# Kernel optimization log

Hardware: AMD Instinct MI355X
Metric: run time of the kernel (lower is better)

Reference implementation:

```python
import jax, jax.numpy as jnp
import numpy as np
from jax.scipy.special import logsumexp

B, L = 32, 128
NEG = -1e9
SPAN_LAMB = 0.5


def setup_inputs() -> dict:
    key = jax.random.key(0)
    ks = jax.random.split(key, 8)
    span_logits = jax.random.normal(ks[0], (B, L, L, 2), jnp.float32)
    ph = jax.random.normal(ks[1], (B, L, L), jnp.float32)
    pt = jax.random.normal(ks[2], (B, L, L), jnp.float32)
    ph_arc = jax.random.normal(ks[3], (B, L, L), jnp.float32)
    spans_ind = jax.random.randint(ks[4], (B, L, L), 0, 3, jnp.int32)
    ph_ind = jax.random.randint(ks[5], (B, L, L), 0, 2, jnp.int32)
    pt_ind = jax.random.randint(ks[6], (B, L, L), 0, 2, jnp.int32)
    lens = jax.random.randint(ks[7], (B,), L // 2, L + 1, jnp.int32)
    i = jnp.arange(L)
    # maskspan[b,i,j] = valid right-closed span i..j within sentence b; row 0 sums to lens
    maskspan = (i[None, :, None] <= i[None, None, :]) & (i[None, None, :] < lens[:, None, None])
    maskarc = (i[None, :, None] < lens[:, None, None]) & (i[None, None, :] < lens[:, None, None])
    return dict(span_logits=span_logits, ph=ph, pt=pt, ph_arc=ph_arc,
                spans_ind=spans_ind, ph_ind=ph_ind, pt_ind=pt_ind,
                maskspan=maskspan, maskarc=maskarc)


def _inside_logZ(span_logits, lens):
    # CYK inside algorithm over right-closed spans; returns sum_b logZ_b.
    scores = logsumexp(span_logits, axis=-1)  # [B,L,L] span score = lse over labels
    Ln = scores.shape[1]
    ar = jnp.arange(Ln)
    # width-0 base: s[i,i] = scores[i,i]
    s0 = jnp.where(jnp.eye(Ln, dtype=bool)[None], scores, NEG)
    li = ar[:, None] + ar[None, :]        # [L,L]: left child right end i+k
    ri = li + 1                           # right child left end i+k+1
    li_c = jnp.clip(li, 0, Ln - 1)
    ri_c = jnp.clip(ri, 0, Ln - 1)

    def step(s, w):
        j = ar + w
        jc = jnp.clip(j, 0, Ln - 1)
        left = s[:, ar[:, None], li_c]                 # [B,L,L] left[b,i,k]=s[b,i,i+k]
        right = s[:, ri_c, jc[:, None]]                # right[b,i,k]=s[b,i+k+1,i+w]
        comb = jnp.where(ar[None, None, :] < w, left + right, NEG)
        new = scores[:, ar, jc] + logsumexp(comb, axis=-1)  # [B,L]
        valid = (j < Ln)[None, :]
        cur = s[:, ar, jc]
        s = s.at[:, ar, jc].set(jnp.where(valid, new, cur))
        return s, None

    s, _ = jax.lax.scan(step, s0, jnp.arange(1, Ln))
    logZ = jnp.take_along_axis(s[:, 0, :], (lens - 1)[:, None], axis=1)[:, 0]
    return logZ.sum()


def _bce_mean(x, y, m):
    # stable BCEWithLogits, mean over masked elements
    l = jnp.maximum(x, 0.0) - x * y + jnp.log1p(jnp.exp(-jnp.abs(x)))
    return jnp.where(m, l, 0.0).sum() / m.sum().astype(jnp.float32)


def reference(span_logits, ph, pt, ph_arc, spans_ind, ph_ind, pt_ind, maskspan, maskarc):
    lens = maskspan[:, 0].sum(-1)                         # [B]
    spans_b = jnp.where(spans_ind > 0, spans_ind - 1, spans_ind).astype(bool)
    # label marginals = d logZ / d span_logits (matches torch autograd-based cyk)
    marginals = jax.grad(_inside_logZ)(span_logits, lens)  # [B,L,L,2]
    pos_mask = maskspan & spans_b
    neg_mask = maskspan & (~spans_b)
    pos_loss = jnp.log(jnp.where(pos_mask, jnp.maximum(marginals[..., 1], 1e-38), 1.0)).sum()
    neg_loss = jnp.log(jnp.where(neg_mask, jnp.maximum(marginals[..., 0], 1e-38), 1.0)).sum()
    loss_spans = -(pos_loss + neg_loss) / lens.sum().astype(jnp.float32)
    loss_ph = _bce_mean(ph, ph_ind.astype(jnp.float32), maskarc)
    loss_pt = _bce_mean(pt, pt_ind.astype(jnp.float32), maskarc)
    return SPAN_LAMB * loss_spans + (1.0 - SPAN_LAMB) * (loss_ph + loss_pt)
```

## Files before the change

### kernel.cpp

```cpp
#include <hip/hip_runtime.h>
#include <hip/hip_bf16.h>
#include <float.h>

#define NB 32
#define NBCE 32
#define L 128
#define NT 1024
#define R 132
#define PAD 40
#define LOGMIN -87.49823f

__device__ __forceinline__ int mask_mode(const void* p) {
    unsigned int v = ((const unsigned int*)p)[0];
    if (v == 1u) return 1;
    if (v == 0x3F800000u) return 2;
    return 0;
}
__device__ __forceinline__ bool mask_at(const void* p, int mode, int idx) {
    if (mode == 1) return ((const int*)p)[idx] != 0;
    if (mode == 2) return ((const float*)p)[idx] != 0.0f;
    return ((const unsigned char*)p)[idx] != 0;
}

__device__ __forceinline__ float lse2(float a, float b) {
    return fmaxf(a, b) + log1pf(__expf(-fabsf(a - b)));
}

template<int C>
__device__ __forceinline__ float dppf(float x) {
    return __int_as_float(__builtin_amdgcn_mov_dpp(__float_as_int(x), C, 0xF, 0xF, true));
}
template<int T>
__device__ __forceinline__ float bfly_max(float x) {
    x = fmaxf(x, dppf<0xB1>(x));
    x = fmaxf(x, dppf<0x4E>(x));
    x = fmaxf(x, dppf<0x141>(x));
    if (T == 16) x = fmaxf(x, dppf<0x140>(x));
    return x;
}
template<int T>
__device__ __forceinline__ float bfly_add(float x) {
    x += dppf<0xB1>(x);
    x += dppf<0x4E>(x);
    x += dppf<0x141>(x);
    if (T == 16) x += dppf<0x140>(x);
    return x;
}

template<int T, int NUMAX>
__device__ __forceinline__ void load_terms(float* v, int sub, int nterm,
                                           const float* p1, const float* p2, float& mloc) {
    p1 += sub; p2 += sub;
#pragma unroll
    for (int kk = 0; kk < NUMAX; kk += 2) {
        if (kk * T >= nterm) break;
        const int o0 = kk * T, o1 = o0 + T;
        float a0 = p1[o0] + p2[o0];
        float a1 = p1[o1] + p2[o1];
        a0 = (sub + o0 < nterm) ? a0 : -FLT_MAX;
        a1 = (sub + o1 < nterm) ? a1 : -FLT_MAX;
        v[kk] = a0; v[kk + 1] = a1;
        mloc = fmaxf(mloc, fmaxf(a0, a1));
    }
}
template<int T, int NUMAX>
__device__ __forceinline__ void sum_exp(const float* v, int nterm, float M, float& s) {
#pragma unroll
    for (int kk = 0; kk < NUMAX; kk += 2) {
        if (kk * T >= nterm) break;
        s += __expf(v[kk] - M) + __expf(v[kk + 1] - M);
    }
}

__global__ __launch_bounds__(NT, 1) void tree_dp_kernel(
    const float* __restrict__ logits,
    const int*   __restrict__ spans_ind,
    const void*  __restrict__ maskspan,
    const float* __restrict__ ph, const float* __restrict__ pt,
    const int* __restrict__ ph_ind, const int* __restrict__ pt_ind,
    const void* __restrict__ maskarc,
    double*      __restrict__ ws)
{
    const int tid = threadIdx.x;

    if (blockIdx.x >= NB) {
        const int mode = mask_mode(maskarc);
        const int tot = NB * L * L;
        double sph = 0.0, spt = 0.0, cnt = 0.0;
        for (int idx = (blockIdx.x - NB) * NT + tid; idx < tot; idx += NBCE * NT) {
            if (mask_at(maskarc, mode, idx)) {
                float x = ph[idx]; float y = (float)ph_ind[idx];
                sph += (double)(fmaxf(x, 0.0f) - x * y + log1pf(__expf(-fabsf(x))));
                x = pt[idx]; y = (float)pt_ind[idx];
                spt += (double)(fmaxf(x, 0.0f) - x * y + log1pf(__expf(-fabsf(x))));
                cnt += 1.0;
            }
        }
        for (int off = 32; off > 0; off >>= 1) {
            sph += __shfl_down(sph, off);
            spt += __shfl_down(spt, off);
            cnt += __shfl_down(cnt, off);
        }
        if ((tid & 63) == 0) {
            atomicAdd(&ws[2], sph); atomicAdd(&ws[3], spt); atomicAdd(&ws[4], cnt);
        }
        return;
    }

    __shared__ float Am[L * R + PAD];
    __shared__ float Gm[L * R + PAD];

    const int b = blockIdx.x;
    const int mbase = b * L * L;
    const int mode = mask_mode(maskspan);

    int pred = (tid < L) && mask_at(maskspan, mode, mbase + tid);
    const int n = __syncthreads_count(pred);

    const float* lg = logits + (size_t)b * L * L * 2;

    for (int e = tid; e < L * L; e += NT) {
        int i = e >> 7, j = e & (L - 1);
        if (i <= j && j < n) {
            const float* p = lg + (size_t)e * 2;
            float v = lse2(p[0], p[1]);
            Am[i * R + j] = v; Am[j * R + i] = v;
            Gm[i * R + j] = v; Gm[j * R + i] = v;
        }
    }
    __syncthreads();

    for (int w = 1; w < n; ++w) {
        int c = n - w;
        if (c > 64) {
            int cell = tid >> 3, sub = tid & 7;
            if (cell < c) {
                int i = cell, j = i + w;
                float v[8]; float mloc = -FLT_MAX;
                load_terms<8, 8>(v, sub, w, &Am[i * R + i], &Am[j * R + i + 1], mloc);
                float M = bfly_max<8>(mloc);
                float s = 0.0f;
                sum_exp<8, 8>(v, w, M, s);
                float S = bfly_add<8>(s);
                if (sub == 0) {
                    float val = Am[i * R + j] + M + __logf(S);
                    Am[i * R + j] = val; Am[j * R + i] = val;
                }
            }
        } else {
            int cell = tid >> 4, sub = tid & 15;
            if (cell < c) {
                int i = cell, j = i + w;
                float v[8]; float mloc = -FLT_MAX;
                load_terms<16, 8>(v, sub, w, &Am[i * R + i], &Am[j * R + i + 1], mloc);
                float M = bfly_max<16>(mloc);
                float s = 0.0f;
                sum_exp<16, 8>(v, w, M, s);
                float S = bfly_add<16>(s);
                if (sub == 0) {
                    float val = Am[i * R + j] + M + __logf(S);
                    Am[i * R + j] = val; Am[j * R + i] = val;
                }
            }
        }
        __syncthreads();
    }

    const float logZ = Am[n - 1];

    for (int w = n - 2; w >= 1; --w) {
        int c = n - w;
        if (c > 64) {
            int cell = tid >> 3, sub = tid & 7;
            if (cell < c) {
                int i = cell, j = i + w;
                int nt1 = n - 1 - j;
                float v1[16], v2[16]; float mloc = -FLT_MAX;
                load_terms<8, 16>(v1, sub, nt1, &Gm[i * R + j + 1], &Am[(j + 1) * R + j + 1], mloc);
                load_terms<8, 16>(v2, sub, i,   &Gm[j * R],         &Am[(i - 1) * R],         mloc);
                float M = bfly_max<8>(mloc);
                float s = 0.0f;
                sum_exp<8, 16>(v1, nt1, M, s);
                sum_exp<8, 16>(v2, i,   M, s);
                float S = bfly_add<8>(s);
                if (sub == 0) {
                    float val = Gm[i * R + j] + M + __logf(S);
                    Gm[i * R + j] = val; Gm[j * R + i] = val;
                }
            }
        } else {
            int cell = tid >> 4, sub = tid & 15;
            if (cell < c) {
                int i = cell, j = i + w;
                int nt1 = n - 1 - j;
                float v1[4], v2[4]; float mloc = -FLT_MAX;
                load_terms<16, 4>(v1, sub, nt1, &Gm[i * R + j + 1], &Am[(j + 1) * R + j + 1], mloc);
                load_terms<16, 4>(v2, sub, i,   &Gm[j * R],         &Am[(i - 1) * R],         mloc);
                float M = bfly_max<16>(mloc);
                float s = 0.0f;
                sum_exp<16, 4>(v1, nt1, M, s);
                sum_exp<16, 4>(v2, i,   M, s);
                float S = bfly_add<16>(s);
                if (sub == 0) {
                    float val = Gm[i * R + j] + M + __logf(S);
                    Gm[i * R + j] = val; Gm[j * R + i] = val;
                }
            }
        }
        __syncthreads();
    }

    const int* si = spans_ind + mbase;
    double local = 0.0;
    {
        int cell = tid >> 3, sub = tid & 7;
        if (cell < n) {
            int i = cell;
            int nt1 = n - 1 - i;
            float v1[16], v2[16]; float mloc = -FLT_MAX;
            load_terms<8, 16>(v1, sub, nt1, &Gm[i * R + i + 1], &Am[(i + 1) * R + i + 1], mloc);
            load_terms<8, 16>(v2, sub, i,   &Gm[i * R],         &Am[(i - 1) * R],         mloc);
            float M = bfly_max<8>(mloc);
            float s = 0.0f;
            sum_exp<8, 16>(v1, nt1, M, s);
            sum_exp<8, 16>(v2, i,   M, s);
            float S = bfly_add<8>(s);
            if (sub == 0) {
                float beta_ii = M + __logf(S);
                const float* p = lg + ((size_t)i * L + i) * 2;
                int ind = si[i * L + i];
                float lc = (ind == 2) ? p[1] : p[0];
                float logm = beta_ii - logZ + lc;
                local += (double)fmaxf(logm, LOGMIN);
            }
        }
    }

    for (int e = tid; e < L * L; e += NT) {
        int i = e >> 7, j = e & (L - 1);
        if (i < j && j < n) {
            const float* p = lg + (size_t)e * 2;
            float a = p[0], cc = p[1];
            float sc = lse2(a, cc);
            int ind = si[e];
            float lc = (ind == 2) ? cc : a;
            float logm = Am[i * R + j] + Gm[i * R + j] - logZ + lc - 2.0f * sc;
            local += (double)fmaxf(logm, LOGMIN);
        }
    }

    for (int off = 32; off > 0; off >>= 1)
        local += __shfl_down(local, off);
    if ((tid & 63) == 0) atomicAdd(&ws[0], local);
    if (tid == 0) atomicAdd(&ws[1], (double)n);
}

__global__ void finalize_kernel(const double* __restrict__ ws, float* __restrict__ out) {
    double loss_spans = -ws[0] / ws[1];
    double bce = (ws[2] + ws[3]) / ws[4];
    out[0] = (float)(0.5 * loss_spans + 0.5 * bce);
}

extern "C" void kernel_launch(void* const* d_in, const int* in_sizes, int n_in,
                              void* d_out, int out_size, void* d_ws, size_t ws_size,
                              hipStream_t stream) {
    (void)in_sizes; (void)n_in; (void)out_size; (void)ws_size;
    const float* span_logits = (const float*)d_in[0];
    const float* ph          = (const float*)d_in[1];
    const float* pt          = (const float*)d_in[2];
    const int*   spans_ind   = (const int*)d_in[4];
    const int*   ph_ind      = (const int*)d_in[5];
    const int*   pt_ind      = (const int*)d_in[6];
    const void*  maskspan    = d_in[7];
    const void*  maskarc     = d_in[8];
    double* ws = (double*)d_ws;
    float* out = (float*)d_out;

    hipMemsetAsync(d_ws, 0, 5 * sizeof(double), stream);
    hipLaunchKernelGGL(tree_dp_kernel, dim3(NB + NBCE), dim3(NT), 0, stream,
                       span_logits, spans_ind, maskspan,
                       ph, pt, ph_ind, pt_ind, maskarc, ws);
    hipLaunchKernelGGL(finalize_kernel, dim3(1), dim3(1), 0, stream, ws, out);
}
```

Before: 324.6 us.

## Software-pipeline inside/outside DP by precomputing next diagonal's partial logsumexp

Restructures the CYK inside and outside diagonal loops so each 8-lane group owns a fixed row i and, during step w, computes the partial logsumexp for its cell on diagonal w+1 from all terms already final, leaving only the one or two terms that depend on the just-written neighbour. The previous value stays in a register and is combined after the barrier. This removes the full reduction from the serial critical path between barriers and merges the root-cell outside step into the loop. It drops the 16-lane mode, so late diagonals use 8 lanes, and the more complex indexing and padding risk correctness.

Result: slower. 343.6 us (+5.8%).

```diff
diff --git a/kernel.cpp b/kernel.cpp
--- a/kernel.cpp
+++ b/kernel.cpp
@@ -7,7 +7,7 @@
 #define L 128
 #define NT 1024
 #define R 132
-#define PAD 40
+#define PAD 160
 #define LOGMIN -87.49823f
 
 __device__ __forceinline__ int mask_mode(const void* p) {
@@ -30,45 +30,42 @@
 __device__ __forceinline__ float dppf(float x) {
     return __int_as_float(__builtin_amdgcn_mov_dpp(__float_as_int(x), C, 0xF, 0xF, true));
 }
-template<int T>
-__device__ __forceinline__ float bfly_max(float x) {
+__device__ __forceinline__ float bfly8_max(float x) {
     x = fmaxf(x, dppf<0xB1>(x));
     x = fmaxf(x, dppf<0x4E>(x));
     x = fmaxf(x, dppf<0x141>(x));
-    if (T == 16) x = fmaxf(x, dppf<0x140>(x));
     return x;
 }
-template<int T>
-__device__ __forceinline__ float bfly_add(float x) {
+__device__ __forceinline__ float bfly8_add(float x) {
     x += dppf<0xB1>(x);
     x += dppf<0x4E>(x);
     x += dppf<0x141>(x);
-    if (T == 16) x += dppf<0x140>(x);
     return x;
 }
 
-template<int T, int NUMAX>
-__device__ __forceinline__ void load_terms(float* v, int sub, int nterm,
+template<int NUMAX>
+__device__ __forceinline__ void load_pairs(float* buf, int sub, int lo, int hi,
                                            const float* p1, const float* p2, float& mloc) {
     p1 += sub; p2 += sub;
 #pragma unroll
     for (int kk = 0; kk < NUMAX; kk += 2) {
-        if (kk * T >= nterm) break;
-        const int o0 = kk * T, o1 = o0 + T;
+        if (kk * 8 >= hi) break;
+        const int o0 = kk * 8, o1 = o0 + 8;
         float a0 = p1[o0] + p2[o0];
         float a1 = p1[o1] + p2[o1];
-        a0 = (sub + o0 < nterm) ? a0 : -FLT_MAX;
-        a1 = (sub + o1 < nterm) ? a1 : -FLT_MAX;
-        v[kk] = a0; v[kk + 1] = a1;
+        const int t0 = sub + o0, t1 = sub + o1;
+        a0 = (t0 >= lo && t0 < hi) ? a0 : -FLT_MAX;
+        a1 = (t1 >= lo && t1 < hi) ? a1 : -FLT_MAX;
+        buf[kk] = a0; buf[kk + 1] = a1;
         mloc = fmaxf(mloc, fmaxf(a0, a1));
     }
 }
-template<int T, int NUMAX>
-__device__ __forceinline__ void sum_exp(const float* v, int nterm, float M, float& s) {
+template<int NUMAX>
+__device__ __forceinline__ void sum_exp8(const float* buf, int hi, float M, float& s) {
 #pragma unroll
     for (int kk = 0; kk < NUMAX; kk += 2) {
-        if (kk * T >= nterm) break;
-        s += __expf(v[kk] - M) + __expf(v[kk + 1] - M);
+        if (kk * 8 >= hi) break;
+        s += __expf(buf[kk] - M) + __expf(buf[kk + 1] - M);
     }
 }
 
@@ -118,133 +115,141 @@
     const int n = __syncthreads_count(pred);
 
     const float* lg = logits + (size_t)b * L * L * 2;
+    const int* si = spans_ind + mbase;
 
     for (int e = tid; e < L * L; e += NT) {
-        int i = e >> 7, j = e & (L - 1);
-        if (i <= j && j < n) {
+        int ii = e >> 7, jj = e & (L - 1);
+        if (ii <= jj && jj < n) {
             const float* p = lg + (size_t)e * 2;
             float v = lse2(p[0], p[1]);
-            Am[i * R + j] = v; Am[j * R + i] = v;
-            Gm[i * R + j] = v; Gm[j * R + i] = v;
+            Am[ii * R + jj] = v; Am[jj * R + ii] = v;
+            Gm[ii * R + jj] = v; Gm[jj * R + ii] = v;
         }
     }
     __syncthreads();
 
+    const int i = tid >> 3;
+    const int sub = tid & 7;
+    double local = 0.0;
+    float buf1[16], buf2[16];
+
+    float ld0 = 0.f, pv = 0.f, scij = 0.f, rjd = 0.f;
+    float m_part = -FLT_MAX, s_part = 0.f;
+    if (i < n) ld0 = Am[i * R + i];
+    if (i < n - 1) scij = Am[i * R + i + 1];
+
     for (int w = 1; w < n; ++w) {
-        int c = n - w;
-        if (c > 64) {
-            int cell = tid >> 3, sub = tid & 7;
-            if (cell < c) {
-                int i = cell, j = i + w;
-                float v[8]; float mloc = -FLT_MAX;
-                load_terms<8, 8>(v, sub, w, &Am[i * R + i], &Am[j * R + i + 1], mloc);
-                float M = bfly_max<8>(mloc);
-                float s = 0.0f;
-                sum_exp<8, 8>(v, w, M, s);
-                float S = bfly_add<8>(s);
-                if (sub == 0) {
-                    float val = Am[i * R + j] + M + __logf(S);
-                    Am[i * R + j] = val; Am[j * R + i] = val;
-                }
-            }
-        } else {
-            int cell = tid >> 4, sub = tid & 15;
-            if (cell < c) {
-                int i = cell, j = i + w;
-                float v[8]; float mloc = -FLT_MAX;
-                load_terms<16, 8>(v, sub, w, &Am[i * R + i], &Am[j * R + i + 1], mloc);
-                float M = bfly_max<16>(mloc);
-                float s = 0.0f;
-                sum_exp<16, 8>(v, w, M, s);
-                float S = bfly_add<16>(s);
-                if (sub == 0) {
-                    float val = Am[i * R + j] + M + __logf(S);
-                    Am[i * R + j] = val; Am[j * R + i] = val;
-                }
-            }
+        const int c = n - w;
+        const int j = i + w;
+        float r0 = 0.f;
+        if (i < c) r0 = Am[j * R + i + 1];
+        float nsc = 0.f, nrjd = 0.f, mloc = -FLT_MAX;
+        const bool pf = (i < c - 1);
+        if (pf) {
+            nsc  = Am[i * R + (j + 1)];
+            nrjd = Am[(j + 1) * R + (j + 1)];
+            load_pairs<16>(buf1, sub, 1, w, &Am[i * R + i], &Am[(j + 1) * R + i + 1], mloc);
+        }
+        if (i < c) {
+            float ta = ld0 + r0;
+            float tb = (w >= 2) ? (pv + rjd) : -FLT_MAX;
+            float M = fmaxf(fmaxf(m_part, ta), tb);
+            float S = s_part * __expf(m_part - M) + __expf(ta - M) + __expf(tb - M);
+            float val = scij + M + __logf(S);
+            if (sub == 0) { Am[i * R + j] = val; Am[j * R + i] = val; }
+            pv = val;
+        }
+        m_part = -FLT_MAX; s_part = 0.f;
+        if (pf) {
+            float Mp = bfly8_max(mloc);
+            float s = 0.f;
+            sum_exp8<16>(buf1, w, Mp, s);
+            s_part = bfly8_add(s);
+            m_part = Mp;
+            scij = nsc; rjd = nrjd;
         }
         __syncthreads();
     }
 
     const float logZ = Am[n - 1];
 
-    for (int w = n - 2; w >= 1; --w) {
-        int c = n - w;
-        if (c > 64) {
-            int cell = tid >> 3, sub = tid & 7;
-            if (cell < c) {
-                int i = cell, j = i + w;
-                int nt1 = n - 1 - j;
-                float v1[16], v2[16]; float mloc = -FLT_MAX;
-                load_terms<8, 16>(v1, sub, nt1, &Gm[i * R + j + 1], &Am[(j + 1) * R + j + 1], mloc);
-                load_terms<8, 16>(v2, sub, i,   &Gm[j * R],         &Am[(i - 1) * R],         mloc);
-                float M = bfly_max<8>(mloc);
-                float s = 0.0f;
-                sum_exp<8, 16>(v1, nt1, M, s);
-                sum_exp<8, 16>(v2, i,   M, s);
-                float S = bfly_add<8>(s);
-                if (sub == 0) {
-                    float val = Gm[i * R + j] + M + __logf(S);
-                    Gm[i * R + j] = val; Gm[j * R + i] = val;
-                }
-            }
-        } else {
-            int cell = tid >> 4, sub = tid & 15;
-            if (cell < c) {
-                int i = cell, j = i + w;
-                int nt1 = n - 1 - j;
-                float v1[4], v2[4]; float mloc = -FLT_MAX;
-                load_terms<16, 4>(v1, sub, nt1, &Gm[i * R + j + 1], &Am[(j + 1) * R + j + 1], mloc);
-                load_terms<16, 4>(v2, sub, i,   &Gm[j * R],         &Am[(i - 1) * R],         mloc);
-                float M = bfly_max<16>(mloc);
-                float s = 0.0f;
-                sum_exp<16, 4>(v1, nt1, M, s);
-                sum_exp<16, 4>(v2, i,   M, s);
-                float S = bfly_add<16>(s);
-                if (sub == 0) {
-                    float val = Gm[i * R + j] + M + __logf(S);
-                    Gm[i * R + j] = val; Gm[j * R + i] = val;
-                }
-            }
-        }
-        __syncthreads();
-    }
-
-    const int* si = spans_ind + mbase;
-    double local = 0.0;
+    float adI = 0.f, adJ = 0.f, scO = 0.f;
+    if (i >= 1 && i < n) adI = Am[(i - 1) * R + (i - 1)];
+    if (i == 0) pv = Gm[n - 1];
+
+    m_part = -FLT_MAX; s_part = 0.f;
     {
-        int cell = tid >> 3, sub = tid & 7;
-        if (cell < n) {
-            int i = cell;
-            int nt1 = n - 1 - i;
-            float v1[16], v2[16]; float mloc = -FLT_MAX;
-            load_terms<8, 16>(v1, sub, nt1, &Gm[i * R + i + 1], &Am[(i + 1) * R + i + 1], mloc);
-            load_terms<8, 16>(v2, sub, i,   &Gm[i * R],         &Am[(i - 1) * R],         mloc);
-            float M = bfly_max<8>(mloc);
-            float s = 0.0f;
-            sum_exp<8, 16>(v1, nt1, M, s);
-            sum_exp<8, 16>(v2, i,   M, s);
-            float S = bfly_add<8>(s);
-            if (sub == 0) {
+        const int w1 = n - 2;
+        if (i < n - w1) {
+            const int j1 = i + w1;
+            scO = Gm[i * R + j1];
+            if (j1 < n - 1) adJ = Am[(j1 + 1) * R + (j1 + 1)];
+            const int nt1 = n - 1 - j1;
+            float mloc = -FLT_MAX;
+            load_pairs<16>(buf1, sub, 1, nt1, &Gm[i * R + j1 + 1], &Am[(j1 + 1) * R + j1 + 1], mloc);
+            load_pairs<16>(buf2, sub, 0, i - 1, &Gm[j1 * R], &Am[(i - 1) * R], mloc);
+            float Mp = bfly8_max(mloc);
+            float s = 0.f;
+            sum_exp8<16>(buf1, nt1, Mp, s);
+            sum_exp8<16>(buf2, i - 1, Mp, s);
+            s_part = bfly8_add(s);
+            m_part = Mp;
+        }
+    }
+
+    for (int w = n - 2; w >= 0; --w) {
+        const int c = n - w;
+        const int j = i + w;
+        float r0g = 0.f;
+        if (i < c && i >= 1) r0g = Gm[j * R + (i - 1)];
+        float nsc = 0.f, nadJ = 0.f, mloc = -FLT_MAX;
+        const bool pf = (w >= 1) && (i < c + 1);
+        int nt1 = 0;
+        if (pf) {
+            const int j1 = i + w - 1;
+            nsc = Gm[i * R + j1];
+            if (j1 < n - 1) nadJ = Am[(j1 + 1) * R + (j1 + 1)];
+            nt1 = n - 1 - j1;
+            load_pairs<16>(buf1, sub, 1, nt1, &Gm[i * R + j1 + 1], &Am[(j1 + 1) * R + j1 + 1], mloc);
+            load_pairs<16>(buf2, sub, 0, i - 1, &Gm[j1 * R], &Am[(i - 1) * R], mloc);
+        }
+        if (i < c) {
+            float g1n = (j < n - 1) ? (pv + adJ) : -FLT_MAX;
+            float g2n = (i >= 1) ? (r0g + adI) : -FLT_MAX;
+            float M = fmaxf(fmaxf(m_part, g1n), g2n);
+            float S = s_part * __expf(m_part - M) + __expf(g1n - M) + __expf(g2n - M);
+            if (w >= 1) {
+                float val = scO + M + __logf(S);
+                if (sub == 0) { Gm[i * R + j] = val; Gm[j * R + i] = val; }
+                pv = val;
+            } else if (sub == 0) {
                 float beta_ii = M + __logf(S);
                 const float* p = lg + ((size_t)i * L + i) * 2;
-                int ind = si[i * L + i];
-                float lc = (ind == 2) ? p[1] : p[0];
-                float logm = beta_ii - logZ + lc;
-                local += (double)fmaxf(logm, LOGMIN);
+                float lc = (si[i * L + i] == 2) ? p[1] : p[0];
+                local += (double)fmaxf(beta_ii - logZ + lc, LOGMIN);
             }
         }
+        m_part = -FLT_MAX; s_part = 0.f;
+        if (pf) {
+            float Mp = bfly8_max(mloc);
+            float s = 0.f;
+            sum_exp8<16>(buf1, nt1, Mp, s);
+            sum_exp8<16>(buf2, i - 1, Mp, s);
+            s_part = bfly8_add(s);
+            m_part = Mp;
+            scO = nsc; adJ = nadJ;
+        }
+        __syncthreads();
     }
 
     for (int e = tid; e < L * L; e += NT) {
-        int i = e >> 7, j = e & (L - 1);
-        if (i < j && j < n) {
+        int ii = e >> 7, jj = e & (L - 1);
+        if (ii < jj && jj < n) {
             const float* p = lg + (size_t)e * 2;
             float a = p[0], cc = p[1];
             float sc = lse2(a, cc);
-            int ind = si[e];
-            float lc = (ind == 2) ? cc : a;
-            float logm = Am[i * R + j] + Gm[i * R + j] - logZ + lc - 2.0f * sc;
+            float lc = (si[e] == 2) ? cc : a;
+            float logm = Am[ii * R + jj] + Gm[ii * R + jj] - logZ + lc - 2.0f * sc;
             local += (double)fmaxf(logm, LOGMIN);
         }
     }
```

## Shift inside-table mirror layout to enable aligned float4 LDS reads in DP

Applied to the files above, without the earlier changes.

Stores the mirrored lower-triangle copy of the inside table shifted by one column so both operands of each split sum share the same column index. That lets the inner loops read aligned float4 blocks from LDS with range masks instead of scalar strided loads. Before the outside pass, a remap step moves the lower triangle back to the unshifted layout, at the cost of an extra pass and two barriers. The outside pass and final marginal pass also switch to the vectorized block loads, and LDS padding is reduced.

Result: slower. 343.6 us (+5.8%).

```diff
diff --git a/kernel.cpp b/kernel.cpp
--- a/kernel.cpp
+++ b/kernel.cpp
@@ -1,5 +1,4 @@
 #include <hip/hip_runtime.h>
-#include <hip/hip_bf16.h>
 #include <float.h>
 
 #define NB 32
@@ -7,7 +6,7 @@
 #define L 128
 #define NT 1024
 #define R 132
-#define PAD 40
+#define PAD 8
 #define LOGMIN -87.49823f
 
 __device__ __forceinline__ int mask_mode(const void* p) {
@@ -47,28 +46,36 @@
     return x;
 }
 
-template<int T, int NUMAX>
-__device__ __forceinline__ void load_terms(float* v, int sub, int nterm,
-                                           const float* p1, const float* p2, float& mloc) {
-    p1 += sub; p2 += sub;
+template<int T, int M>
+__device__ __forceinline__ void load_blk(float4* buf, int sub, int clo, int chi,
+                                         const float* p1, const float* p2, float& mloc) {
+    const int kb0 = clo >> 2;
 #pragma unroll
-    for (int kk = 0; kk < NUMAX; kk += 2) {
-        if (kk * T >= nterm) break;
-        const int o0 = kk * T, o1 = o0 + T;
-        float a0 = p1[o0] + p2[o0];
-        float a1 = p1[o1] + p2[o1];
-        a0 = (sub + o0 < nterm) ? a0 : -FLT_MAX;
-        a1 = (sub + o1 < nterm) ? a1 : -FLT_MAX;
-        v[kk] = a0; v[kk + 1] = a1;
-        mloc = fmaxf(mloc, fmaxf(a0, a1));
-    }
-}
-template<int T, int NUMAX>
-__device__ __forceinline__ void sum_exp(const float* v, int nterm, float M, float& s) {
+    for (int m = 0; m < M; ++m) {
+        const int c0 = (kb0 + sub + T * m) << 2;
+        if (c0 >= chi) break;
+        const float4 a = *(const float4*)(p1 + c0);
+        const float4 b = *(const float4*)(p2 + c0);
+        const unsigned rng = (unsigned)(chi - clo);
+        float4 v;
+        v.x = ((unsigned)(c0 + 0 - clo) < rng) ? a.x + b.x : -FLT_MAX;
+        v.y = ((unsigned)(c0 + 1 - clo) < rng) ? a.y + b.y : -FLT_MAX;
+        v.z = ((unsigned)(c0 + 2 - clo) < rng) ? a.z + b.z : -FLT_MAX;
+        v.w = ((unsigned)(c0 + 3 - clo) < rng) ? a.w + b.w : -FLT_MAX;
+        buf[m] = v;
+        mloc = fmaxf(mloc, fmaxf(fmaxf(v.x, v.y), fmaxf(v.z, v.w)));
+    }
+}
+template<int T, int M>
+__device__ __forceinline__ void sumexp_blk(const float4* buf, int sub, int clo, int chi,
+                                           float Mv, float& s) {
+    const int kb0 = clo >> 2;
 #pragma unroll
-    for (int kk = 0; kk < NUMAX; kk += 2) {
-        if (kk * T >= nterm) break;
-        s += __expf(v[kk] - M) + __expf(v[kk + 1] - M);
+    for (int m = 0; m < M; ++m) {
+        const int c0 = (kb0 + sub + T * m) << 2;
+        if (c0 >= chi) break;
+        const float4 v = buf[m];
+        s += __expf(v.x - Mv) + __expf(v.y - Mv) + __expf(v.z - Mv) + __expf(v.w - Mv);
     }
 }
 
@@ -107,59 +114,63 @@
         return;
     }
 
-    __shared__ float Am[L * R + PAD];
-    __shared__ float Gm[L * R + PAD];
+    __shared__ __align__(16) float Am[L * R + PAD];
+    __shared__ __align__(16) float Gm[L * R + PAD];
 
     const int b = blockIdx.x;
     const int mbase = b * L * L;
     const int mode = mask_mode(maskspan);
 
-    int pred = (tid < L) && mask_at(maskspan, mode, mbase + tid);
-    const int n = __syncthreads_count(pred);
+    int predv = (tid < L) && mask_at(maskspan, mode, mbase + tid);
+    const int n = __syncthreads_count(predv);
 
     const float* lg = logits + (size_t)b * L * L * 2;
+    const int* si = spans_ind + mbase;
 
     for (int e = tid; e < L * L; e += NT) {
-        int i = e >> 7, j = e & (L - 1);
-        if (i <= j && j < n) {
+        int ii = e >> 7, jj = e & (L - 1);
+        if (ii <= jj && jj < n) {
             const float* p = lg + (size_t)e * 2;
             float v = lse2(p[0], p[1]);
-            Am[i * R + j] = v; Am[j * R + i] = v;
-            Gm[i * R + j] = v; Gm[j * R + i] = v;
+            Am[ii * R + jj] = v;
+            if (ii >= 1) Am[jj * R + ii - 1] = v;
+            Gm[ii * R + jj] = v; Gm[jj * R + ii] = v;
         }
     }
     __syncthreads();
 
     for (int w = 1; w < n; ++w) {
-        int c = n - w;
+        const int c = n - w;
         if (c > 64) {
-            int cell = tid >> 3, sub = tid & 7;
+            const int cell = tid >> 3, sub = tid & 7;
             if (cell < c) {
-                int i = cell, j = i + w;
-                float v[8]; float mloc = -FLT_MAX;
-                load_terms<8, 8>(v, sub, w, &Am[i * R + i], &Am[j * R + i + 1], mloc);
-                float M = bfly_max<8>(mloc);
+                const int i = cell, j = i + w;
+                float4 buf[3]; float mloc = -FLT_MAX;
+                load_blk<8, 3>(buf, sub, i, j, &Am[i * R], &Am[j * R], mloc);
+                float Mv = bfly_max<8>(mloc);
                 float s = 0.0f;
-                sum_exp<8, 8>(v, w, M, s);
+                sumexp_blk<8, 3>(buf, sub, i, j, Mv, s);
                 float S = bfly_add<8>(s);
                 if (sub == 0) {
-                    float val = Am[i * R + j] + M + __logf(S);
-                    Am[i * R + j] = val; Am[j * R + i] = val;
+                    float val = Am[i * R + j] + Mv + __logf(S);
+                    Am[i * R + j] = val;
+                    Am[j * R + i - 1] = val;
                 }
             }
         } else {
-            int cell = tid >> 4, sub = tid & 15;
+            const int cell = tid >> 4, sub = tid & 15;
             if (cell < c) {
-                int i = cell, j = i + w;
-                float v[8]; float mloc = -FLT_MAX;
-                load_terms<16, 8>(v, sub, w, &Am[i * R + i], &Am[j * R + i + 1], mloc);
-                float M = bfly_max<16>(mloc);
+                const int i = cell, j = i + w;
+                float4 buf[2]; float mloc = -FLT_MAX;
+                load_blk<16, 2>(buf, sub, i, j, &Am[i * R], &Am[j * R], mloc);
+                float Mv = bfly_max<16>(mloc);
                 float s = 0.0f;
-                sum_exp<16, 8>(v, w, M, s);
+                sumexp_blk<16, 2>(buf, sub, i, j, Mv, s);
                 float S = bfly_add<16>(s);
                 if (sub == 0) {
-                    float val = Am[i * R + j] + M + __logf(S);
-                    Am[i * R + j] = val; Am[j * R + i] = val;
+                    float val = Am[i * R + j] + Mv + __logf(S);
+                    Am[i * R + j] = val;
+                    Am[j * R + i - 1] = val;
                 }
             }
         }
@@ -168,41 +179,61 @@
 
     const float logZ = Am[n - 1];
 
+    {
+        float tmp[16];
+#pragma unroll
+        for (int p = 0; p < 16; ++p) {
+            const int e = tid + p * NT;
+            const int r = e >> 7, cc = e & (L - 1);
+            tmp[p] = 0.0f;
+            if (cc < r && r < n)
+                tmp[p] = (cc == 0) ? Am[r] : Am[r * R + cc - 1];
+        }
+        __syncthreads();
+#pragma unroll
+        for (int p = 0; p < 16; ++p) {
+            const int e = tid + p * NT;
+            const int r = e >> 7, cc = e & (L - 1);
+            if (cc < r && r < n) Am[r * R + cc] = tmp[p];
+        }
+    }
+    __syncthreads();
+
     for (int w = n - 2; w >= 1; --w) {
-        int c = n - w;
+        const int c = n - w;
         if (c > 64) {
-            int cell = tid >> 3, sub = tid & 7;
+            const int cell = tid >> 3, sub = tid & 7;
             if (cell < c) {
-                int i = cell, j = i + w;
-                int nt1 = n - 1 - j;
-                float v1[16], v2[16]; float mloc = -FLT_MAX;
-                load_terms<8, 16>(v1, sub, nt1, &Gm[i * R + j + 1], &Am[(j + 1) * R + j + 1], mloc);
-                load_terms<8, 16>(v2, sub, i,   &Gm[j * R],         &Am[(i - 1) * R],         mloc);
-                float M = bfly_max<8>(mloc);
+                const int i = cell, j = i + w;
+                float4 b1[4], b2[4]; float mloc = -FLT_MAX;
+                load_blk<8, 4>(b1, sub, j + 1, n, &Gm[i * R], &Am[(j + 1) * R], mloc);
+                const float* pa2 = &Am[(i >= 1 ? i - 1 : 0) * R];
+                load_blk<8, 4>(b2, sub, 0, i, &Gm[j * R], pa2, mloc);
+                float Mv = bfly_max<8>(mloc);
                 float s = 0.0f;
-                sum_exp<8, 16>(v1, nt1, M, s);
-                sum_exp<8, 16>(v2, i,   M, s);
+                sumexp_blk<8, 4>(b1, sub, j + 1, n, Mv, s);
+                sumexp_blk<8, 4>(b2, sub, 0, i, Mv, s);
                 float S = bfly_add<8>(s);
                 if (sub == 0) {
-                    float val = Gm[i * R + j] + M + __logf(S);
+                    float val = Gm[i * R + j] + Mv + __logf(S);
                     Gm[i * R + j] = val; Gm[j * R + i] = val;
                 }
             }
         } else {
-            int cell = tid >> 4, sub = tid & 15;
+            const int cell = tid >> 4, sub = tid & 15;
             if (cell < c) {
-                int i = cell, j = i + w;
-                int nt1 = n - 1 - j;
-                float v1[4], v2[4]; float mloc = -FLT_MAX;
-                load_terms<16, 4>(v1, sub, nt1, &Gm[i * R + j + 1], &Am[(j + 1) * R + j + 1], mloc);
-                load_terms<16, 4>(v2, sub, i,   &Gm[j * R],         &Am[(i - 1) * R],         mloc);
-                float M = bfly_max<16>(mloc);
+                const int i = cell, j = i + w;
+                float4 b1[2], b2[1]; float mloc = -FLT_MAX;
+                load_blk<16, 2>(b1, sub, j + 1, n, &Gm[i * R], &Am[(j + 1) * R], mloc);
+                const float* pa2 = &Am[(i >= 1 ? i - 1 : 0) * R];
+                load_blk<16, 1>(b2, sub, 0, i, &Gm[j * R], pa2, mloc);
+                float Mv = bfly_max<16>(mloc);
                 float s = 0.0f;
-                sum_exp<16, 4>(v1, nt1, M, s);
-                sum_exp<16, 4>(v2, i,   M, s);
+                sumexp_blk<16, 2>(b1, sub, j + 1, n, Mv, s);
+                sumexp_blk<16, 1>(b2, sub, 0, i, Mv, s);
                 float S = bfly_add<16>(s);
                 if (sub == 0) {
-                    float val = Gm[i * R + j] + M + __logf(S);
+                    float val = Gm[i * R + j] + Mv + __logf(S);
                     Gm[i * R + j] = val; Gm[j * R + i] = val;
                 }
             }
@@ -210,41 +241,38 @@
         __syncthreads();
     }
 
-    const int* si = spans_ind + mbase;
     double local = 0.0;
     {
-        int cell = tid >> 3, sub = tid & 7;
+        const int cell = tid >> 3, sub = tid & 7;
         if (cell < n) {
-            int i = cell;
-            int nt1 = n - 1 - i;
-            float v1[16], v2[16]; float mloc = -FLT_MAX;
-            load_terms<8, 16>(v1, sub, nt1, &Gm[i * R + i + 1], &Am[(i + 1) * R + i + 1], mloc);
-            load_terms<8, 16>(v2, sub, i,   &Gm[i * R],         &Am[(i - 1) * R],         mloc);
-            float M = bfly_max<8>(mloc);
+            const int i = cell;
+            float4 b1[4], b2[4]; float mloc = -FLT_MAX;
+            const float* pa1 = &Am[(i + 1 < n ? i + 1 : 0) * R];
+            load_blk<8, 4>(b1, sub, i + 1, n, &Gm[i * R], pa1, mloc);
+            const float* pa2 = &Am[(i >= 1 ? i - 1 : 0) * R];
+            load_blk<8, 4>(b2, sub, 0, i, &Gm[i * R], pa2, mloc);
+            float Mv = bfly_max<8>(mloc);
             float s = 0.0f;
-            sum_exp<8, 16>(v1, nt1, M, s);
-            sum_exp<8, 16>(v2, i,   M, s);
+            sumexp_blk<8, 4>(b1, sub, i + 1, n, Mv, s);
+            sumexp_blk<8, 4>(b2, sub, 0, i, Mv, s);
             float S = bfly_add<8>(s);
             if (sub == 0) {
-                float beta_ii = M + __logf(S);
+                float beta_ii = Mv + __logf(S);
                 const float* p = lg + ((size_t)i * L + i) * 2;
-                int ind = si[i * L + i];
-                float lc = (ind == 2) ? p[1] : p[0];
-                float logm = beta_ii - logZ + lc;
-                local += (double)fmaxf(logm, LOGMIN);
+                float lc = (si[i * L + i] == 2) ? p[1] : p[0];
+                local += (double)fmaxf(beta_ii - logZ + lc, LOGMIN);
             }
         }
     }
 
     for (int e = tid; e < L * L; e += NT) {
-        int i = e >> 7, j = e & (L - 1);
-        if (i < j && j < n) {
+        int ii = e >> 7, jj = e & (L - 1);
+        if (ii < jj && jj < n) {
             const float* p = lg + (size_t)e * 2;
             float a = p[0], cc = p[1];
             float sc = lse2(a, cc);
-            int ind = si[e];
-            float lc = (ind == 2) ? cc : a;
-            float logm = Am[i * R + j] + Gm[i * R + j] - logZ + lc - 2.0f * sc;
+            float lc = (si[e] == 2) ? cc : a;
+            float logm = Am[ii * R + jj] + Gm[ii * R + jj] - logZ + lc - 2.0f * sc;
             local += (double)fmaxf(logm, LOGMIN);
         }
     }
```

## Shrink DP blocks to 256 threads, each octet looping over several cells

Applied to the files above, without the earlier changes.

Cuts the block from 1024 to 256 threads. Each 8-lane subgroup now processes up to four DP cells per anti-diagonal, using a fixed 8-lane reduction in place of the earlier switch between 8-lane and 16-lane groups. The aim is cheaper __syncthreads barriers across the long serial width loop and less idle-lane overhead. The cost is less parallelism per diagonal for wide diagonals, plus a longer per-thread serial loop, and the BCE blocks also run with fewer threads.

Measured after the change: 514.2 us. 1.58x slower.

```diff
diff --git a/kernel.cpp b/kernel.cpp
--- a/kernel.cpp
+++ b/kernel.cpp
@@ -1,11 +1,10 @@
 #include <hip/hip_runtime.h>
-#include <hip/hip_bf16.h>
 #include <float.h>
 
 #define NB 32
 #define NBCE 32
 #define L 128
-#define NT 1024
+#define NT 256
 #define R 132
 #define PAD 40
 #define LOGMIN -87.49823f
@@ -30,31 +29,27 @@
 __device__ __forceinline__ float dppf(float x) {
     return __int_as_float(__builtin_amdgcn_mov_dpp(__float_as_int(x), C, 0xF, 0xF, true));
 }
-template<int T>
-__device__ __forceinline__ float bfly_max(float x) {
+__device__ __forceinline__ float bfly_max8(float x) {
     x = fmaxf(x, dppf<0xB1>(x));
     x = fmaxf(x, dppf<0x4E>(x));
     x = fmaxf(x, dppf<0x141>(x));
-    if (T == 16) x = fmaxf(x, dppf<0x140>(x));
     return x;
 }
-template<int T>
-__device__ __forceinline__ float bfly_add(float x) {
+__device__ __forceinline__ float bfly_add8(float x) {
     x += dppf<0xB1>(x);
     x += dppf<0x4E>(x);
     x += dppf<0x141>(x);
-    if (T == 16) x += dppf<0x140>(x);
     return x;
 }
 
-template<int T, int NUMAX>
+template<int NUMAX>
 __device__ __forceinline__ void load_terms(float* v, int sub, int nterm,
                                            const float* p1, const float* p2, float& mloc) {
     p1 += sub; p2 += sub;
 #pragma unroll
     for (int kk = 0; kk < NUMAX; kk += 2) {
-        if (kk * T >= nterm) break;
-        const int o0 = kk * T, o1 = o0 + T;
+        if (kk * 8 >= nterm) break;
+        const int o0 = kk * 8, o1 = o0 + 8;
         float a0 = p1[o0] + p2[o0];
         float a1 = p1[o1] + p2[o1];
         a0 = (sub + o0 < nterm) ? a0 : -FLT_MAX;
@@ -63,11 +58,11 @@
         mloc = fmaxf(mloc, fmaxf(a0, a1));
     }
 }
-template<int T, int NUMAX>
-__device__ __forceinline__ void sum_exp(const float* v, int nterm, float M, float& s) {
+template<int NUMAX>
+__device__ __forceinline__ void sum_exp8(const float* v, int nterm, float M, float& s) {
 #pragma unroll
     for (int kk = 0; kk < NUMAX; kk += 2) {
-        if (kk * T >= nterm) break;
+        if (kk * 8 >= nterm) break;
         s += __expf(v[kk] - M) + __expf(v[kk + 1] - M);
     }
 }
@@ -107,8 +102,8 @@
         return;
     }
 
-    __shared__ float Am[L * R + PAD];
-    __shared__ float Gm[L * R + PAD];
+    __shared__ __align__(16) float Am[L * R + PAD];
+    __shared__ __align__(16) float Gm[L * R + PAD];
 
     const int b = blockIdx.x;
     const int mbase = b * L * L;
@@ -118,6 +113,7 @@
     const int n = __syncthreads_count(pred);
 
     const float* lg = logits + (size_t)b * L * L * 2;
+    const int* si = spans_ind + mbase;
 
     for (int e = tid; e < L * L; e += NT) {
         int i = e >> 7, j = e & (L - 1);
@@ -130,109 +126,75 @@
     }
     __syncthreads();
 
+    const int sg = tid >> 3, sub = tid & 7;
+
     for (int w = 1; w < n; ++w) {
-        int c = n - w;
-        if (c > 64) {
-            int cell = tid >> 3, sub = tid & 7;
-            if (cell < c) {
-                int i = cell, j = i + w;
-                float v[8]; float mloc = -FLT_MAX;
-                load_terms<8, 8>(v, sub, w, &Am[i * R + i], &Am[j * R + i + 1], mloc);
-                float M = bfly_max<8>(mloc);
-                float s = 0.0f;
-                sum_exp<8, 8>(v, w, M, s);
-                float S = bfly_add<8>(s);
-                if (sub == 0) {
-                    float val = Am[i * R + j] + M + __logf(S);
-                    Am[i * R + j] = val; Am[j * R + i] = val;
-                }
+        const int c = n - w;
+#pragma unroll
+        for (int q = 0; q < 4; ++q) {
+            const int i = sg + (q << 5);
+            if (i >= c) break;
+            const int j = i + w;
+            float v[16]; float mloc = -FLT_MAX;
+            load_terms<16>(v, sub, w, &Am[i * R + i], &Am[j * R + i + 1], mloc);
+            float M = bfly_max8(mloc);
+            float s = 0.0f;
+            sum_exp8<16>(v, w, M, s);
+            float S = bfly_add8(s);
+            if (sub == 0) {
+                float val = Am[i * R + j] + M + __logf(S);
+                Am[i * R + j] = val; Am[j * R + i] = val;
             }
-        } else {
-            int cell = tid >> 4, sub = tid & 15;
-            if (cell < c) {
-                int i = cell, j = i + w;
-                float v[8]; float mloc = -FLT_MAX;
-                load_terms<16, 8>(v, sub, w, &Am[i * R + i], &Am[j * R + i + 1], mloc);
-                float M = bfly_max<16>(mloc);
-                float s = 0.0f;
-                sum_exp<16, 8>(v, w, M, s);
-                float S = bfly_add<16>(s);
-                if (sub == 0) {
-                    float val = Am[i * R + j] + M + __logf(S);
-                    Am[i * R + j] = val; Am[j * R + i] = val;
-                }
+        }
+        __syncthreads();
+    }
+
+    const float logZ = Am[n - 1];
+
+    for (int w = n - 2; w >= 1; --w) {
+        const int c = n - w;
+#pragma unroll
+        for (int q = 0; q < 4; ++q) {
+            const int i = sg + (q << 5);
+            if (i >= c) break;
+            const int j = i + w;
+            const int nt1 = n - 1 - j;
+            float v1[16], v2[16]; float mloc = -FLT_MAX;
+            load_terms<16>(v1, sub, nt1, &Gm[i * R + j + 1], &Am[(j + 1) * R + j + 1], mloc);
+            load_terms<16>(v2, sub, i,   &Gm[j * R],         &Am[(i - 1) * R],         mloc);
+            float M = bfly_max8(mloc);
+            float s = 0.0f;
+            sum_exp8<16>(v1, nt1, M, s);
+            sum_exp8<16>(v2, i,   M, s);
+            float S = bfly_add8(s);
+            if (sub == 0) {
+                float val = Gm[i * R + j] + M + __logf(S);
+                Gm[i * R + j] = val; Gm[j * R + i] = val;
             }
         }
         __syncthreads();
     }
 
-    const float logZ = Am[n - 1];
-
-    for (int w = n - 2; w >= 1; --w) {
-        int c = n - w;
-        if (c > 64) {
-            int cell = tid >> 3, sub = tid & 7;
-            if (cell < c) {
-                int i = cell, j = i + w;
-                int nt1 = n - 1 - j;
-                float v1[16], v2[16]; float mloc = -FLT_MAX;
-                load_terms<8, 16>(v1, sub, nt1, &Gm[i * R + j + 1], &Am[(j + 1) * R + j + 1], mloc);
-                load_terms<8, 16>(v2, sub, i,   &Gm[j * R],         &Am[(i - 1) * R],         mloc);
-                float M = bfly_max<8>(mloc);
-                float s = 0.0f;
-                sum_exp<8, 16>(v1, nt1, M, s);
-                sum_exp<8, 16>(v2, i,   M, s);
-                float S = bfly_add<8>(s);
-                if (sub == 0) {
-                    float val = Gm[i * R + j] + M + __logf(S);
-                    Gm[i * R + j] = val; Gm[j * R + i] = val;
-                }
-            }
-        } else {
-            int cell = tid >> 4, sub = tid & 15;
-            if (cell < c) {
-                int i = cell, j = i + w;
-                int nt1 = n - 1 - j;
-                float v1[4], v2[4]; float mloc = -FLT_MAX;
-                load_terms<16, 4>(v1, sub, nt1, &Gm[i * R + j + 1], &Am[(j + 1) * R + j + 1], mloc);
-                load_terms<16, 4>(v2, sub, i,   &Gm[j * R],         &Am[(i - 1) * R],         mloc);
-                float M = bfly_max<16>(mloc);
-                float s = 0.0f;
-                sum_exp<16, 4>(v1, nt1, M, s);
-                sum_exp<16, 4>(v2, i,   M, s);
-                float S = bfly_add<16>(s);
-                if (sub == 0) {
-                    float val = Gm[i * R + j] + M + __logf(S);
-                    Gm[i * R + j] = val; Gm[j * R + i] = val;
-                }
-            }
-        }
-        __syncthreads();
-    }
-
-    const int* si = spans_ind + mbase;
     double local = 0.0;
-    {
-        int cell = tid >> 3, sub = tid & 7;
-        if (cell < n) {
-            int i = cell;
-            int nt1 = n - 1 - i;
-            float v1[16], v2[16]; float mloc = -FLT_MAX;
-            load_terms<8, 16>(v1, sub, nt1, &Gm[i * R + i + 1], &Am[(i + 1) * R + i + 1], mloc);
-            load_terms<8, 16>(v2, sub, i,   &Gm[i * R],         &Am[(i - 1) * R],         mloc);
-            float M = bfly_max<8>(mloc);
-            float s = 0.0f;
-            sum_exp<8, 16>(v1, nt1, M, s);
-            sum_exp<8, 16>(v2, i,   M, s);
-            float S = bfly_add<8>(s);
-            if (sub == 0) {
-                float beta_ii = M + __logf(S);
-                const float* p = lg + ((size_t)i * L + i) * 2;
-                int ind = si[i * L + i];
-                float lc = (ind == 2) ? p[1] : p[0];
-                float logm = beta_ii - logZ + lc;
-                local += (double)fmaxf(logm, LOGMIN);
-            }
+#pragma unroll
+    for (int q = 0; q < 4; ++q) {
+        const int i = sg + (q << 5);
+        if (i >= n) break;
+        const int nt1 = n - 1 - i;
+        float v1[16], v2[16]; float mloc = -FLT_MAX;
+        load_terms<16>(v1, sub, nt1, &Gm[i * R + i + 1], &Am[(i + 1) * R + i + 1], mloc);
+        load_terms<16>(v2, sub, i,   &Gm[i * R],         &Am[(i - 1) * R],         mloc);
+        float M = bfly_max8(mloc);
+        float s = 0.0f;
+        sum_exp8<16>(v1, nt1, M, s);
+        sum_exp8<16>(v2, i,   M, s);
+        float S = bfly_add8(s);
+        if (sub == 0) {
+            float beta_ii = M + __logf(S);
+            const float* p = lg + ((size_t)i * L + i) * 2;
+            int ind = si[i * L + i];
+            float lc = (ind == 2) ? p[1] : p[0];
+            local += (double)fmaxf(beta_ii - logZ + lc, LOGMIN);
         }
     }
 
```
